# Performance work log

Measured on AMD Instinct MI355X. Metric: run time of the kernel, lower is better.

The kernel has to match this reference:

```python
import jax, jax.numpy as jnp
import numpy as np


def setup_inputs() -> dict:
    key = jax.random.key(0)
    k1, k2 = jax.random.split(key)
    B, D, F, T = 4, 64, 64, 2000
    x = jax.random.normal(k1, (B, D, F, T), dtype=jnp.float32)
    e = jax.random.normal(k2, (B, D, F), dtype=jnp.float32)
    return {"x": x, "e": e}


def _pos_encoding(T, DF, dtype):
    # sinusoidal PE, interleaved sin (even dims) / cos (odd dims)
    pos = jnp.arange(T, dtype=dtype)[:, None]                      # (T, 1)
    div = jnp.exp(jnp.arange(0, DF, 2, dtype=dtype)
                  * (-jnp.log(jnp.asarray(10000.0, dtype)) / DF))  # (DF/2,)
    pe = jnp.zeros((T, DF), dtype)
    pe = pe.at[:, 0::2].set(jnp.sin(pos * div))
    pe = pe.at[:, 1::2].set(jnp.cos(pos * div))
    return pe


def reference(x, e):
    # x: (B, D, F, T), e: (B, D, F)
    B, D, nF, T = x.shape
    DF = D * nF
    # q: broadcast e over time, flatten (D,F) -> DF, add sinusoidal PE
    q = e.reshape(B, 1, DF) + _pos_encoding(T, DF, x.dtype)        # (B, T, DF)
    k = x.reshape(B, DF, T)                                        # (B, DF, T)
    v = jnp.swapaxes(k, 1, 2)                                      # (B, T, DF)
    scale = jnp.sqrt(jnp.asarray(DF, x.dtype))
    scores = jax.nn.softmax(jnp.matmul(q, k) / scale, axis=-1)     # (B, T, T)
    att = jnp.matmul(scores, v)                                    # (B, T, DF)
    return jnp.swapaxes(att, 1, 2).reshape(B, D, nF, T)            # (B, D, F, T)
```

## Files before the change

### kernel.cpp

```cpp
#include <hip/hip_runtime.h>
#include <stdint.h>

#define TR  2000
#define TP  2048
#define NDF 4096
#define NB  4

typedef __attribute__((ext_vector_type(8))) short short8;
typedef __attribute__((ext_vector_type(4))) float f32x4;

static __device__ __forceinline__ unsigned short f2bf(float f) {
  union { float f; unsigned u; } v; v.f = f;
  return (unsigned short)((v.u + 0x7fffu + ((v.u >> 16) & 1u)) >> 16);
}

typedef const __attribute__((address_space(1))) void CGV;
typedef __attribute__((address_space(3))) void LV;

static __device__ __forceinline__ void async16(const void* g, void* l) {
  __builtin_amdgcn_global_load_lds((CGV*)g, (LV*)l, 16, 0, 0);
}

__global__ void k_prep_xv(const float* __restrict__ x,
                          unsigned short* __restrict__ Xb,
                          unsigned short* __restrict__ Vb) {
  __shared__ float tile[32][33];
  const int b  = blockIdx.z;
  const int d0 = blockIdx.x * 32;
  const int t0 = blockIdx.y * 32;
  const int lx = threadIdx.x & 31;
  const int ly = threadIdx.x >> 5;
#pragma unroll
  for (int i = 0; i < 4; ++i) {
    const int d = d0 + ly + i * 8;
    const int t = t0 + lx;
    float v = 0.f;
    if (t < TR) v = x[((size_t)b * NDF + d) * TR + t];
    tile[ly + i * 8][lx] = v;
    Xb[((size_t)b * NDF + d) * TP + t] = f2bf(v);
  }
  __syncthreads();
#pragma unroll
  for (int i = 0; i < 4; ++i) {
    const int t = t0 + ly + i * 8;
    const int d = d0 + lx;
    Vb[((size_t)b * TP + t) * NDF + d] = f2bf(tile[lx][ly + i * 8]);
  }
}

__global__ void k_prep_q(const float* __restrict__ e,
                         unsigned short* __restrict__ Qb) {
  const int gid = blockIdx.x * 256 + threadIdx.x;
  const int t   = gid >> 9;
  const int d0  = (gid & 511) * 8;
  float pe[8];
#pragma unroll
  for (int p = 0; p < 4; ++p) {
    const float twoi = (float)(d0 + 2 * p);
    const float dv   = expf(twoi * (-9.210340371976184f / 4096.0f));
    const float ang  = (float)t * dv;
    pe[2 * p]     = sinf(ang);
    pe[2 * p + 1] = cosf(ang);
  }
#pragma unroll
  for (int b = 0; b < NB; ++b) {
    const float* ep = e + (size_t)b * NDF + d0;
    short8 sv;
#pragma unroll
    for (int j = 0; j < 8; ++j) sv[j] = (short)f2bf(ep[j] + pe[j]);
    *(short8*)(Qb + ((size_t)b * TP + t) * NDF + d0) = sv;
  }
}

template <int LDK, bool GUARD>
__launch_bounds__(512, 2)
__global__ void k_gemm256(const unsigned short* __restrict__ A,
                          const unsigned short* __restrict__ Bt,
                          float* __restrict__ C,
                          size_t sA, size_t sB, size_t sC,
                          int ldc, int ncols) {
  __shared__ unsigned short lds[65536];
  constexpr int NT = LDK / 64;
  const int b  = blockIdx.z;
  const int m0 = blockIdx.x * 256;
  const int n0 = blockIdx.y * 256;
  const unsigned short* Ab = A + (size_t)b * sA;
  const unsigned short* Bb = Bt + (size_t)b * sB;
  const int t = threadIdx.x, w = t >> 6, l = t & 63;
  const int wm = w >> 2, wn = w & 3;
  const int lr = l & 15, lg = l >> 4;

  const int rofs = w * 8 + (l >> 3);
  const int csw  = ((l & 7) ^ ((l >> 3) & 7)) * 8;
  const unsigned short* gA = Ab + (size_t)(m0 + rofs) * LDK + csw;
  const unsigned short* gB = Bb + (size_t)(n0 + rofs) * LDK + csw;

#define STAGE(c, isB, h, kt) do {                                            \
    const unsigned short* _g = ((isB) ? gB : gA)                             \
                               + (size_t)((h) * 128) * LDK + (size_t)(kt) * 64; \
    unsigned short* _d = lds + (c) * 32768 + (isB) * 16384 + (h) * 8192      \
                         + w * 512;                                          \
    async16(_g, _d);                                                         \
    async16(_g + (size_t)64 * LDK, _d + 4096);                               \
  } while (0)

  const unsigned short* laA[2] = { lds + wm * 8192 + lr * 64,
                                   lds + 32768 + wm * 8192 + lr * 64 };
  const unsigned short* lbB[2] = { lds + 16384 + (wn >> 1) * 8192 + ((wn & 1) * 64 + lr) * 64,
                                   lds + 49152 + (wn >> 1) * 8192 + ((wn & 1) * 64 + lr) * 64 };
  const int s0 = ((0 + lg) ^ (lr & 7)) * 8;
  const int s1 = ((4 + lg) ^ (lr & 7)) * 8;

#define PB do { asm volatile("" ::: "memory");                               \
                __builtin_amdgcn_s_barrier();                                \
                asm volatile("" ::: "memory"); } while (0)
#define VMC(n) asm volatile("s_waitcnt vmcnt(" #n ")" ::: "memory")
#define RD_A(base, off) do {                                                 \
    _Pragma("unroll")                                                        \
    for (int f = 0; f < 4; ++f) {                                            \
      af[f][0] = *(const short8*)((base) + ((off) + f) * 1024 + s0);         \
      af[f][1] = *(const short8*)((base) + ((off) + f) * 1024 + s1);         \
    } } while (0)
#define RD_B(dst, base, off) do {                                            \
    _Pragma("unroll")                                                        \
    for (int f = 0; f < 2; ++f) {                                            \
      dst[f][0] = *(const short8*)((base) + ((off) + f) * 1024 + s0);        \
      dst[f][1] = *(const short8*)((base) + ((off) + f) * 1024 + s1);        \
    } } while (0)
#define MM(I0, J0, BFV) do {                                                 \
    __builtin_amdgcn_s_setprio(1);                                           \
    _Pragma("unroll")                                                        \
    for (int i = 0; i < 4; ++i)                                              \
      _Pragma("unroll")                                                      \
      for (int j = 0; j < 2; ++j) {                                          \
        acc[(I0) + i][(J0) + j] = __builtin_amdgcn_mfma_f32_16x16x32_bf16(   \
            af[i][0], BFV[j][0], acc[(I0) + i][(J0) + j], 0, 0, 0);          \
        acc[(I0) + i][(J0) + j] = __builtin_amdgcn_mfma_f32_16x16x32_bf16(   \
            af[i][1], BFV[j][1], acc[(I0) + i][(J0) + j], 0, 0, 0);          \
      }                                                                      \
    __builtin_amdgcn_s_setprio(0); } while (0)

  short8 af[4][2], bf01[2][2], bf23[2][2];
  f32x4 acc[8][4] = {};

  STAGE(0, 0, 0, 0); STAGE(0, 0, 1, 0); STAGE(0, 1, 0, 0); STAGE(0, 1, 1, 0);
  STAGE(1, 1, 0, 1); STAGE(1, 1, 1, 1);
  VMC(4);
  PB;
  RD_B(bf01, lbB[0], 0);

  for (int i2 = 0; i2 < NT / 2; ++i2) {
    const int kt0 = 2 * i2, kt1 = kt0 + 1;
    const bool pf = (kt0 + 2 < NT);

    RD_A(laA[0], 0);
    STAGE(1, 0, 0, kt1);
    MM(0, 0, bf01);
    PB;

    RD_B(bf23, lbB[0], 2);
    STAGE(1, 0, 1, kt1);
    MM(0, 2, bf23);
    PB;

    RD_A(laA[0], 4);
    if (pf) STAGE(0, 1, 0, kt0 + 2);
    MM(4, 0, bf01);
    if (pf) VMC(6); else VMC(0);
    PB;

    RD_B(bf01, lbB[1], 0);
    if (pf) STAGE(0, 1, 1, kt0 + 2);
    MM(4, 2, bf23);
    if (pf) VMC(4); else VMC(0);
    PB;

    RD_A(laA[1], 0);
    if (pf) STAGE(0, 0, 0, kt0 + 2);
    MM(0, 0, bf01);
    PB;

    RD_B(bf23, lbB[1], 2);
    if (pf) STAGE(0, 0, 1, kt0 + 2);
    MM(0, 2, bf23);
    PB;

    RD_A(laA[1], 4);
    if (pf) STAGE(1, 1, 0, kt1 + 2);
    MM(4, 0, bf01);
    if (pf) VMC(6);
    PB;

    if (pf) RD_B(bf01, lbB[0], 0);
    if (pf) STAGE(1, 1, 1, kt1 + 2);
    MM(4, 2, bf23);
    if (pf) VMC(4);
    PB;
  }
#undef STAGE
#undef RD_A
#undef RD_B
#undef MM
#undef PB
#undef VMC

  float* Cb = C + (size_t)b * sC;
#pragma unroll
  for (int i = 0; i < 8; ++i) {
    const int rb = m0 + wm * 128 + i * 16 + lg * 4;
#pragma unroll
    for (int f = 0; f < 4; ++f) {
      const int cg = n0 + wn * 64 + f * 16 + lr;
      if (!GUARD || cg < ncols) {
#pragma unroll
        for (int j = 0; j < 4; ++j)
          Cb[(size_t)(rb + j) * ldc + cg] = acc[i][f][j];
      }
    }
  }
}

__global__ void k_softmax(const float* __restrict__ S,
                          unsigned short* __restrict__ P) {
  const int i = blockIdx.x;
  const int b = blockIdx.y;
  unsigned short* prow = P + ((size_t)b * TP + i) * TP;
  const int t = threadIdx.x;
  if (i >= TR) {
    for (int j = t; j < TP; j += 256) prow[j] = 0;
    return;
  }
  const float* srow = S + ((size_t)b * TP + i) * TP;
  float v[8];
  float mx = -1e30f;
#pragma unroll
  for (int r = 0; r < 8; ++r) {
    const int j = t + r * 256;
    const float s = (j < TR) ? srow[j] * 0.015625f : -1e30f;
    v[r] = s;
    mx = fmaxf(mx, s);
  }
  __shared__ float red[4];
#pragma unroll
  for (int off = 32; off > 0; off >>= 1) mx = fmaxf(mx, __shfl_xor(mx, off));
  if ((t & 63) == 0) red[t >> 6] = mx;
  __syncthreads();
  mx = fmaxf(fmaxf(red[0], red[1]), fmaxf(red[2], red[3]));
  __syncthreads();
  float sum = 0.f;
#pragma unroll
  for (int r = 0; r < 8; ++r) {
    const float ev = __expf(v[r] - mx);
    v[r] = ev;
    sum += ev;
  }
#pragma unroll
  for (int off = 32; off > 0; off >>= 1) sum += __shfl_xor(sum, off);
  if ((t & 63) == 0) red[t >> 6] = sum;
  __syncthreads();
  sum = red[0] + red[1] + red[2] + red[3];
  const float inv = 1.f / sum;
#pragma unroll
  for (int r = 0; r < 8; ++r) {
    const int j = t + r * 256;
    prow[j] = (j < TR) ? f2bf(v[r] * inv) : (unsigned short)0;
  }
}

extern "C" void kernel_launch(void* const* d_in, const int* in_sizes, int n_in,
                              void* d_out, int out_size, void* d_ws, size_t ws_size,
                              hipStream_t stream) {
  const float* x = (const float*)d_in[0];
  const float* e = (const float*)d_in[1];
  float* out = (float*)d_out;
  char* ws = (char*)d_ws;

  const size_t szQ = (size_t)NB * TP * NDF * 2;
  const size_t szV = szQ;
  const size_t szX = szQ;
  const size_t szS = (size_t)NB * TP * TP * 4;
  const size_t szP = (size_t)NB * TP * TP * 2;
  if (ws_size < szQ + szV + szX + szS + szP) return;

  unsigned short* Qb = (unsigned short*)(ws);
  unsigned short* Vb = (unsigned short*)(ws + szQ);
  unsigned short* Xb = (unsigned short*)(ws + szQ + szV);
  float*          S  = (float*)(ws + szQ + szV + szX);
  unsigned short* P  = (unsigned short*)(ws + szQ + szV + szX + szS);

  k_prep_xv<<<dim3(NDF / 32, TP / 32, NB), 256, 0, stream>>>(x, Xb, Vb);
  k_prep_q<<<dim3((TP * (NDF / 8)) / 256), 256, 0, stream>>>(e, Qb);
  k_gemm256<NDF, false><<<dim3(TP / 256, TP / 256, NB), 512, 0, stream>>>(
      Qb, Vb, S,
      (size_t)TP * NDF, (size_t)TP * NDF, (size_t)TP * TP, TP, TP);
  k_softmax<<<dim3(TP, NB), 256, 0, stream>>>(S, P);
  k_gemm256<TP, true><<<dim3(NDF / 256, TP / 256, NB), 512, 0, stream>>>(
      Xb, P, out,
      (size_t)NDF * TP, (size_t)TP * TP, (size_t)NDF * TR, TR, TR);
}
```

Before: 335.5 us.

## Restructure GEMM main loop with double-buffered A fragments and sched barriers

```diff
diff --git a/kernel.cpp b/kernel.cpp
--- a/kernel.cpp
+++ b/kernel.cpp
@@ -95,31 +95,29 @@
   const unsigned short* gA = Ab + (size_t)(m0 + rofs) * LDK + csw;
   const unsigned short* gB = Bb + (size_t)(n0 + rofs) * LDK + csw;
 
-#define STAGE(c, isB, h, kt) do {                                            \
+#define STAGE(cb, isB, h, kt) do {                                           \
     const unsigned short* _g = ((isB) ? gB : gA)                             \
                                + (size_t)((h) * 128) * LDK + (size_t)(kt) * 64; \
-    unsigned short* _d = lds + (c) * 32768 + (isB) * 16384 + (h) * 8192      \
-                         + w * 512;                                          \
+    unsigned short* _d = lds + (cb) + (isB) * 16384 + (h) * 8192 + w * 512;  \
     async16(_g, _d);                                                         \
     async16(_g + (size_t)64 * LDK, _d + 4096);                               \
   } while (0)
 
-  const unsigned short* laA[2] = { lds + wm * 8192 + lr * 64,
-                                   lds + 32768 + wm * 8192 + lr * 64 };
-  const unsigned short* lbB[2] = { lds + 16384 + (wn >> 1) * 8192 + ((wn & 1) * 64 + lr) * 64,
-                                   lds + 49152 + (wn >> 1) * 8192 + ((wn & 1) * 64 + lr) * 64 };
   const int s0 = ((0 + lg) ^ (lr & 7)) * 8;
   const int s1 = ((4 + lg) ^ (lr & 7)) * 8;
+  const int aoff = wm * 8192 + lr * 64;
+  const int boff = 16384 + (wn >> 1) * 8192 + ((wn & 1) * 64 + lr) * 64;
 
 #define PB do { asm volatile("" ::: "memory");                               \
                 __builtin_amdgcn_s_barrier();                                \
                 asm volatile("" ::: "memory"); } while (0)
+#define SCHED0 __builtin_amdgcn_sched_barrier(0)
 #define VMC(n) asm volatile("s_waitcnt vmcnt(" #n ")" ::: "memory")
-#define RD_A(base, off) do {                                                 \
+#define RD_A(dst, base, off) do {                                            \
     _Pragma("unroll")                                                        \
     for (int f = 0; f < 4; ++f) {                                            \
-      af[f][0] = *(const short8*)((base) + ((off) + f) * 1024 + s0);         \
-      af[f][1] = *(const short8*)((base) + ((off) + f) * 1024 + s1);         \
+      dst[f][0] = *(const short8*)((base) + ((off) + f) * 1024 + s0);        \
+      dst[f][1] = *(const short8*)((base) + ((off) + f) * 1024 + s1);        \
     } } while (0)
 #define RD_B(dst, base, off) do {                                            \
     _Pragma("unroll")                                                        \
@@ -127,81 +125,78 @@
       dst[f][0] = *(const short8*)((base) + ((off) + f) * 1024 + s0);        \
       dst[f][1] = *(const short8*)((base) + ((off) + f) * 1024 + s1);        \
     } } while (0)
-#define MM(I0, J0, BFV) do {                                                 \
+#define MM(I0, J0, AFV, BFV) do {                                            \
     __builtin_amdgcn_s_setprio(1);                                           \
     _Pragma("unroll")                                                        \
     for (int i = 0; i < 4; ++i)                                              \
       _Pragma("unroll")                                                      \
       for (int j = 0; j < 2; ++j) {                                          \
         acc[(I0) + i][(J0) + j] = __builtin_amdgcn_mfma_f32_16x16x32_bf16(   \
-            af[i][0], BFV[j][0], acc[(I0) + i][(J0) + j], 0, 0, 0);          \
+            AFV[i][0], BFV[j][0], acc[(I0) + i][(J0) + j], 0, 0, 0);         \
         acc[(I0) + i][(J0) + j] = __builtin_amdgcn_mfma_f32_16x16x32_bf16(   \
-            af[i][1], BFV[j][1], acc[(I0) + i][(J0) + j], 0, 0, 0);          \
+            AFV[i][1], BFV[j][1], acc[(I0) + i][(J0) + j], 0, 0, 0);         \
       }                                                                      \
     __builtin_amdgcn_s_setprio(0); } while (0)
 
-  short8 af[4][2], bf01[2][2], bf23[2][2];
+  short8 afLo[4][2], afHi[4][2], bf01[2][2], bf23[2][2];
   f32x4 acc[8][4] = {};
 
-  STAGE(0, 0, 0, 0); STAGE(0, 0, 1, 0); STAGE(0, 1, 0, 0); STAGE(0, 1, 1, 0);
-  STAGE(1, 1, 0, 1); STAGE(1, 1, 1, 1);
-  VMC(4);
+  STAGE(0, 0, 0, 0);
+  STAGE(0, 0, 1, 0);
+  STAGE(0, 1, 0, 0);
+  STAGE(0, 1, 1, 0);
+  STAGE(32768, 0, 0, 1);
+  STAGE(32768, 1, 0, 1);
+  STAGE(32768, 1, 1, 1);
+  VMC(6);
   PB;
-  RD_B(bf01, lbB[0], 0);
-
-  for (int i2 = 0; i2 < NT / 2; ++i2) {
-    const int kt0 = 2 * i2, kt1 = kt0 + 1;
-    const bool pf = (kt0 + 2 < NT);
-
-    RD_A(laA[0], 0);
-    STAGE(1, 0, 0, kt1);
-    MM(0, 0, bf01);
-    PB;
-
-    RD_B(bf23, lbB[0], 2);
-    STAGE(1, 0, 1, kt1);
-    MM(0, 2, bf23);
-    PB;
-
-    RD_A(laA[0], 4);
-    if (pf) STAGE(0, 1, 0, kt0 + 2);
-    MM(4, 0, bf01);
-    if (pf) VMC(6); else VMC(0);
-    PB;
-
-    RD_B(bf01, lbB[1], 0);
-    if (pf) STAGE(0, 1, 1, kt0 + 2);
-    MM(4, 2, bf23);
-    if (pf) VMC(4); else VMC(0);
-    PB;
-
-    RD_A(laA[1], 0);
-    if (pf) STAGE(0, 0, 0, kt0 + 2);
-    MM(0, 0, bf01);
-    PB;
-
-    RD_B(bf23, lbB[1], 2);
-    if (pf) STAGE(0, 0, 1, kt0 + 2);
-    MM(0, 2, bf23);
-    PB;
-
-    RD_A(laA[1], 4);
-    if (pf) STAGE(1, 1, 0, kt1 + 2);
-    MM(4, 0, bf01);
-    if (pf) VMC(6);
-    PB;
-
-    if (pf) RD_B(bf01, lbB[0], 0);
-    if (pf) STAGE(1, 1, 1, kt1 + 2);
-    MM(4, 2, bf23);
-    if (pf) VMC(4);
-    PB;
-  }
+  RD_B(bf01, lds + boff, 0);
+  RD_A(afLo, lds + aoff, 0);
+  SCHED0;
+
+  auto ktile = [&](int kt, bool nx, bool pf2) __attribute__((always_inline)) {
+    const int cb  = (kt & 1) << 15;
+    const int cbn = cb ^ 32768;
+    const unsigned short* la  = lds + cb  + aoff;
+    const unsigned short* lb  = lds + cb  + boff;
+    const unsigned short* laN = lds + cbn + aoff;
+    const unsigned short* lbN = lds + cbn + boff;
+
+    RD_B(bf23, lb, 2);
+    RD_A(afHi, la, 4);
+    if (nx) STAGE(cbn, 0, 1, kt + 1);
+    SCHED0;
+    MM(0, 0, afLo, bf01);
+    PB;
+
+    SCHED0;
+    MM(0, 2, afLo, bf23);
+    if (nx) VMC(0);
+    PB;
+
+    if (nx) RD_A(afLo, laN, 0);
+    if (pf2) STAGE(cb, 1, 0, kt + 2);
+    SCHED0;
+    MM(4, 0, afHi, bf01);
+    PB;
+
+    if (nx) RD_B(bf01, lbN, 0);
+    if (pf2) { STAGE(cb, 0, 0, kt + 2); STAGE(cb, 1, 1, kt + 2); }
+    SCHED0;
+    MM(4, 2, afHi, bf23);
+    PB;
+  };
+
+  for (int kt = 0; kt < NT - 2; ++kt) ktile(kt, true, true);
+  ktile(NT - 2, true, false);
+  ktile(NT - 1, false, false);
+
 #undef STAGE
 #undef RD_A
 #undef RD_B
 #undef MM
 #undef PB
+#undef SCHED0
 #undef VMC
 
   float* Cb = C + (size_t)b * sC;
```

Result: slower. 370.2 us (+10.3%).

## Split query into shared PE matrix plus per-batch e·x bias term

Applied to the files above, without the earlier changes.

```diff
diff --git a/kernel.cpp b/kernel.cpp
--- a/kernel.cpp
+++ b/kernel.cpp
@@ -22,14 +22,18 @@
 }
 
 __global__ void k_prep_xv(const float* __restrict__ x,
+                          const float* __restrict__ e,
                           unsigned short* __restrict__ Xb,
-                          unsigned short* __restrict__ Vb) {
+                          unsigned short* __restrict__ Vb,
+                          float* __restrict__ up) {
   __shared__ float tile[32][33];
+  __shared__ float ured[8][32];
   const int b  = blockIdx.z;
   const int d0 = blockIdx.x * 32;
   const int t0 = blockIdx.y * 32;
   const int lx = threadIdx.x & 31;
   const int ly = threadIdx.x >> 5;
+  float us = 0.f;
 #pragma unroll
   for (int i = 0; i < 4; ++i) {
     const int d = d0 + ly + i * 8;
@@ -38,7 +42,9 @@
     if (t < TR) v = x[((size_t)b * NDF + d) * TR + t];
     tile[ly + i * 8][lx] = v;
     Xb[((size_t)b * NDF + d) * TP + t] = f2bf(v);
-  }
+    us += e[(size_t)b * NDF + d] * v;
+  }
+  ured[ly][lx] = us;
   __syncthreads();
 #pragma unroll
   for (int i = 0; i < 4; ++i) {
@@ -46,30 +52,36 @@
     const int d = d0 + lx;
     Vb[((size_t)b * TP + t) * NDF + d] = f2bf(tile[lx][ly + i * 8]);
   }
-}
-
-__global__ void k_prep_q(const float* __restrict__ e,
-                         unsigned short* __restrict__ Qb) {
+  if (threadIdx.x < 32) {
+    float s = 0.f;
+#pragma unroll
+    for (int r = 0; r < 8; ++r) s += ured[r][threadIdx.x];
+    up[(size_t)blockIdx.x * (NB * TP) + (size_t)b * TP + t0 + threadIdx.x] = s;
+  }
+}
+
+__global__ void k_sum_u(const float* __restrict__ up, float* __restrict__ u) {
+  const int idx = blockIdx.x * 256 + threadIdx.x;
+  float s = 0.f;
+#pragma unroll 8
+  for (int i = 0; i < NDF / 32; ++i) s += up[(size_t)i * (NB * TP) + idx];
+  u[idx] = s;
+}
+
+__global__ void k_prep_pe(unsigned short* __restrict__ PEb) {
   const int gid = blockIdx.x * 256 + threadIdx.x;
   const int t   = gid >> 9;
   const int d0  = (gid & 511) * 8;
-  float pe[8];
+  short8 sv;
 #pragma unroll
   for (int p = 0; p < 4; ++p) {
     const float twoi = (float)(d0 + 2 * p);
     const float dv   = expf(twoi * (-9.210340371976184f / 4096.0f));
     const float ang  = (float)t * dv;
-    pe[2 * p]     = sinf(ang);
-    pe[2 * p + 1] = cosf(ang);
-  }
-#pragma unroll
-  for (int b = 0; b < NB; ++b) {
-    const float* ep = e + (size_t)b * NDF + d0;
-    short8 sv;
-#pragma unroll
-    for (int j = 0; j < 8; ++j) sv[j] = (short)f2bf(ep[j] + pe[j]);
-    *(short8*)(Qb + ((size_t)b * TP + t) * NDF + d0) = sv;
-  }
+    sv[2 * p]     = (short)f2bf(sinf(ang));
+    sv[2 * p + 1] = (short)f2bf(cosf(ang));
+  }
+  *(short8*)(PEb + (size_t)t * NDF + d0) = sv;
 }
 
 template <int LDK, bool GUARD>
@@ -157,40 +169,33 @@
     STAGE(1, 0, 0, kt1);
     MM(0, 0, bf01);
     PB;
-
     RD_B(bf23, lbB[0], 2);
     STAGE(1, 0, 1, kt1);
     MM(0, 2, bf23);
     PB;
-
     RD_A(laA[0], 4);
     if (pf) STAGE(0, 1, 0, kt0 + 2);
     MM(4, 0, bf01);
     if (pf) VMC(6); else VMC(0);
     PB;
-
     RD_B(bf01, lbB[1], 0);
     if (pf) STAGE(0, 1, 1, kt0 + 2);
     MM(4, 2, bf23);
     if (pf) VMC(4); else VMC(0);
     PB;
-
     RD_A(laA[1], 0);
     if (pf) STAGE(0, 0, 0, kt0 + 2);
     MM(0, 0, bf01);
     PB;
-
     RD_B(bf23, lbB[1], 2);
     if (pf) STAGE(0, 0, 1, kt0 + 2);
     MM(0, 2, bf23);
     PB;
-
     RD_A(laA[1], 4);
     if (pf) STAGE(1, 1, 0, kt1 + 2);
     MM(4, 0, bf01);
     if (pf) VMC(6);
     PB;
-
     if (pf) RD_B(bf01, lbB[0], 0);
     if (pf) STAGE(1, 1, 1, kt1 + 2);
     MM(4, 2, bf23);
@@ -221,6 +226,7 @@
 }
 
 __global__ void k_softmax(const float* __restrict__ S,
+                          const float* __restrict__ u,
                           unsigned short* __restrict__ P) {
   const int i = blockIdx.x;
   const int b = blockIdx.y;
@@ -231,12 +237,13 @@
     return;
   }
   const float* srow = S + ((size_t)b * TP + i) * TP;
+  const float* ub   = u + (size_t)b * TP;
   float v[8];
   float mx = -1e30f;
 #pragma unroll
   for (int r = 0; r < 8; ++r) {
     const int j = t + r * 256;
-    const float s = (j < TR) ? srow[j] * 0.015625f : -1e30f;
+    const float s = (j < TR) ? (srow[j] + ub[j]) * 0.015625f : -1e30f;
     v[r] = s;
     mx = fmaxf(mx, s);
   }
@@ -275,25 +282,30 @@
   float* out = (float*)d_out;
   char* ws = (char*)d_ws;
 
-  const size_t szQ = (size_t)NB * TP * NDF * 2;
-  const size_t szV = szQ;
-  const size_t szX = szQ;
-  const size_t szS = (size_t)NB * TP * TP * 4;
-  const size_t szP = (size_t)NB * TP * TP * 2;
-  if (ws_size < szQ + szV + szX + szS + szP) return;
-
-  unsigned short* Qb = (unsigned short*)(ws);
-  unsigned short* Vb = (unsigned short*)(ws + szQ);
-  unsigned short* Xb = (unsigned short*)(ws + szQ + szV);
-  float*          S  = (float*)(ws + szQ + szV + szX);
-  unsigned short* P  = (unsigned short*)(ws + szQ + szV + szX + szS);
-
-  k_prep_xv<<<dim3(NDF / 32, TP / 32, NB), 256, 0, stream>>>(x, Xb, Vb);
-  k_prep_q<<<dim3((TP * (NDF / 8)) / 256), 256, 0, stream>>>(e, Qb);
+  const size_t szPE = (size_t)TP * NDF * 2;
+  const size_t szV  = (size_t)NB * TP * NDF * 2;
+  const size_t szX  = szV;
+  const size_t szS  = (size_t)NB * TP * TP * 4;
+  const size_t szP  = (size_t)NB * TP * TP * 2;
+  const size_t szUP = (size_t)(NDF / 32) * NB * TP * 4;
+  const size_t szU  = (size_t)NB * TP * 4;
+  if (ws_size < szPE + szV + szX + szS + szP + szUP + szU) return;
+
+  unsigned short* PEb = (unsigned short*)(ws);
+  unsigned short* Vb  = (unsigned short*)(ws + szPE);
+  unsigned short* Xb  = (unsigned short*)(ws + szPE + szV);
+  float*          S   = (float*)(ws + szPE + szV + szX);
+  unsigned short* P   = (unsigned short*)(ws + szPE + szV + szX + szS);
+  float*          up  = (float*)(ws + szPE + szV + szX + szS + szP);
+  float*          u   = (float*)(ws + szPE + szV + szX + szS + szP + szUP);
+
+  k_prep_xv<<<dim3(NDF / 32, TP / 32, NB), 256, 0, stream>>>(x, e, Xb, Vb, up);
+  k_sum_u<<<dim3(NB * TP / 256), 256, 0, stream>>>(up, u);
+  k_prep_pe<<<dim3((TP * (NDF / 8)) / 256), 256, 0, stream>>>(PEb);
   k_gemm256<NDF, false><<<dim3(TP / 256, TP / 256, NB), 512, 0, stream>>>(
-      Qb, Vb, S,
-      (size_t)TP * NDF, (size_t)TP * NDF, (size_t)TP * TP, TP, TP);
-  k_softmax<<<dim3(TP, NB), 256, 0, stream>>>(S, P);
+      PEb, Vb, S,
+      0, (size_t)TP * NDF, (size_t)TP * TP, TP, TP);
+  k_softmax<<<dim3(TP, NB), 256, 0, stream>>>(S, u, P);
   k_gemm256<TP, true><<<dim3(NDF / 256, TP / 256, NB), 512, 0, stream>>>(
       Xb, P, out,
       (size_t)NDF * TP, (size_t)TP * TP, (size_t)NDF * TR, TR, TR);
```

Measured after the change: 340.5 us. No clear change (+1.5%).
